# Kernel tuning notes

Measured on AMD Instinct MI355X. Metric: run time of the kernel, lower is better.

Reference implementation:

```python
import jax, jax.numpy as jnp
import numpy as np

NEG_SLOPE = 0.2

def leaky(x):
    return jnp.where(x >= 0, x, NEG_SLOPE * x)

def setup_inputs() -> dict:
    key = jax.random.key(0)
    ks = jax.random.split(key, 9)
    B, D, H = 2048, 128, 512
    s = lambda fan: 1.0 / np.sqrt(fan)
    return {
        "x":   jax.random.normal(ks[0], (B, D), jnp.float32),
        "We1": jax.random.normal(ks[1], (H, D), jnp.float32) * s(D),
        "be1": jax.random.normal(ks[2], (H,), jnp.float32) * s(D),
        "We2": jax.random.normal(ks[3], (D, H), jnp.float32) * s(H),
        "be2": jax.random.normal(ks[4], (D,), jnp.float32) * s(H),
        "W1s": jax.random.normal(ks[5], (D, H), jnp.float32),      # dec_j.linear1 weight (H,1) stacked -> (D,H)
        "b1s": jax.random.normal(ks[6], (D, H), jnp.float32) * 0.1,
        "W2s": jax.random.normal(ks[7], (D, D, H), jnp.float32) * s(H),  # dec_j.linear2 weight (D,H) stacked
        "b2s": jax.random.normal(ks[8], (D, D), jnp.float32) * s(H),
    }

def reference(x, We1, be1, We2, be2, W1s, b1s, W2s, b2s):
    # Encoder: D -> H -> D, tanh
    enc_h = leaky(x @ We1.T + be1)                     # (B,H)
    encoded = jnp.tanh(enc_h @ We2.T + be2)            # (B,D)
    # Per-feature decoders, vectorized over j: dec_j(encoded[:, j])
    z = encoded.T                                      # (D,B) latent scalar per decoder j
    hid = leaky(z[:, :, None] * W1s[:, None, :] + b1s[:, None, :])   # (D,B,H)
    terms = jnp.einsum('jbh,jdh->jbd', hid, W2s) + b2s[:, None, :]   # (D,B,D)
    # outputs[i] = sum_{j<=i} terms[j] -> inclusive prefix sum over j
    outputs = jnp.tanh(jnp.cumsum(terms, axis=0))      # (D,B,D)
    return outputs
```

## Files before the change

### kernel.cpp

```cpp
#include <hip/hip_runtime.h>

#define B_SZ 2048
#define D_SZ 128
#define H_SZ 512
#define JC 8
#define NCH 16
#define CPG 3
#define NGRP 5

typedef _Float16 half8 __attribute__((ext_vector_type(8)));
typedef float floatx4 __attribute__((ext_vector_type(4)));
typedef unsigned int uint4v __attribute__((ext_vector_type(4)));

static __device__ __forceinline__ float tanh_fast(float x) {
  float e = __expf(2.0f * x);
  return 1.0f - 2.0f * __builtin_amdgcn_rcpf(e + 1.0f);
}

static __device__ __forceinline__ void split_pair(float a, float b,
                                                  unsigned int& hi,
                                                  unsigned int& lo) {
  auto h = __builtin_amdgcn_cvt_pkrtz(a, b);
  float ra = a - (float)h[0];
  float rb = b - (float)h[1];
  auto l = __builtin_amdgcn_cvt_pkrtz(ra, rb);
  hi = __builtin_bit_cast(unsigned int, h);
  lo = __builtin_bit_cast(unsigned int, l);
}

__global__ __launch_bounds__(256) void split_w2_kernel(
    const float* __restrict__ W2s, _Float16* __restrict__ W2h,
    _Float16* __restrict__ W2l) {
  const int idx = blockIdx.x * 256 + threadIdx.x;
  const int dl = idx & 63, kg = (idx >> 6) & 63, dtj = idx >> 12;
  const int d = (dtj & 1) * 64 + dl, j = dtj >> 1;
  const float* src = W2s + ((size_t)j * D_SZ + d) * H_SZ + kg * 8;
  float4 a = *(const float4*)src;
  float4 b = *(const float4*)(src + 4);
  unsigned int h0, l0, h1, l1, h2, l2, h3, l3;
  split_pair(a.x, a.y, h0, l0); split_pair(a.z, a.w, h1, l1);
  split_pair(b.x, b.y, h2, l2); split_pair(b.z, b.w, h3, l3);
  ((uint4*)W2h)[idx] = make_uint4(h0, h1, h2, h3);
  ((uint4*)W2l)[idx] = make_uint4(l0, l1, l2, l3);
}

__global__ __launch_bounds__(256) void enc_kernel(
    const float* __restrict__ x, const float* __restrict__ We1,
    const float* __restrict__ be1, const float* __restrict__ We2,
    const float* __restrict__ be2, float* __restrict__ z) {
  __shared__ float xs[8][132];
  __shared__ float hs[8][516];
  const int t = threadIdx.x;
  const int b0 = blockIdx.x * 8;
  {
    int r = t >> 5, c4 = t & 31;
    float4 v = ((const float4*)(x + (size_t)(b0 + r) * D_SZ))[c4];
    xs[r][c4 * 4 + 0] = v.x; xs[r][c4 * 4 + 1] = v.y;
    xs[r][c4 * 4 + 2] = v.z; xs[r][c4 * 4 + 3] = v.w;
  }
  __syncthreads();
  for (int hb = 0; hb < 2; ++hb) {
    const int h = t + hb * 256;
    float acc[8];
    float bias = be1[h];
#pragma unroll
    for (int r = 0; r < 8; ++r) acc[r] = bias;
    const float4* wp = (const float4*)(We1 + (size_t)h * D_SZ);
    for (int k4 = 0; k4 < 32; ++k4) {
      float4 wv = wp[k4];
#pragma unroll
      for (int r = 0; r < 8; ++r) {
        acc[r] = fmaf(wv.x, xs[r][k4 * 4 + 0], acc[r]);
        acc[r] = fmaf(wv.y, xs[r][k4 * 4 + 1], acc[r]);
        acc[r] = fmaf(wv.z, xs[r][k4 * 4 + 2], acc[r]);
        acc[r] = fmaf(wv.w, xs[r][k4 * 4 + 3], acc[r]);
      }
    }
#pragma unroll
    for (int r = 0; r < 8; ++r) {
      float u = acc[r];
      hs[r][h] = fmaxf(u, 0.2f * u);
    }
  }
  __syncthreads();
  {
    const int d = t & 127, rg = t >> 7;
    float acc[4];
    float bias = be2[d];
#pragma unroll
    for (int r = 0; r < 4; ++r) acc[r] = bias;
    const float4* wp = (const float4*)(We2 + (size_t)d * H_SZ);
    for (int k4 = 0; k4 < 128; ++k4) {
      float4 wv = wp[k4];
#pragma unroll
      for (int r = 0; r < 4; ++r) {
        int row = rg * 4 + r;
        acc[r] = fmaf(wv.x, hs[row][k4 * 4 + 0], acc[r]);
        acc[r] = fmaf(wv.y, hs[row][k4 * 4 + 1], acc[r]);
        acc[r] = fmaf(wv.z, hs[row][k4 * 4 + 2], acc[r]);
        acc[r] = fmaf(wv.w, hs[row][k4 * 4 + 3], acc[r]);
      }
    }
#pragma unroll
    for (int r = 0; r < 4; ++r) {
      z[(size_t)d * B_SZ + b0 + rg * 4 + r] = tanh_fast(acc[r]);
    }
  }
}

__global__ __launch_bounds__(256, 4) void dec_kernel(
    const float* __restrict__ W1s, const float* __restrict__ b1s,
    const _Float16* __restrict__ W2h, const _Float16* __restrict__ W2l,
    const float* __restrict__ b2s, const float* __restrict__ z,
    float* __restrict__ out, float* __restrict__ T) {
  __shared__ float w1L[JC][512];
  __shared__ float b1L[JC][512];
  __shared__ float zL[JC][64];
  __shared__ float b2L[JC][64];

  const int t = threadIdx.x, bx = blockIdx.x;
  const int cohort = bx & 31, bt = bx >> 5;
  const int dt = cohort & 1, jc = cohort >> 1;
  const int b0 = bt * 64, d0 = dt * 64, j0 = jc * JC;

#pragma unroll
  for (int i = 0; i < 4; ++i) {
    int g = t + 256 * i;
    int jr = g >> 7, col = (g & 127) * 4;
    *(float4*)&w1L[jr][col] = *(const float4*)(W1s + (size_t)(j0 + jr) * H_SZ + col);
    *(float4*)&b1L[jr][col] = *(const float4*)(b1s + (size_t)(j0 + jr) * H_SZ + col);
  }
  if (t < 128) {
    int jr = t >> 4, col = (t & 15) * 4;
    *(float4*)&zL[jr][col]  = *(const float4*)(z   + (size_t)(j0 + jr) * B_SZ + b0 + col);
    *(float4*)&b2L[jr][col] = *(const float4*)(b2s + (size_t)(j0 + jr) * D_SZ + d0 + col);
  }
  __syncthreads();

  const int lane = t & 63;
  const int quad = lane >> 4, l16 = lane & 15;
  const int wb = (t >> 6) & 1, wd = t >> 7;
  const int brow0 = wb * 32 + l16;

  floatx4 acc[2][2][3];
#pragma unroll
  for (int a = 0; a < 2; ++a)
#pragma unroll
    for (int b = 0; b < 2; ++b)
#pragma unroll
      for (int p = 0; p < 3; ++p) acc[a][b][p] = (floatx4){0.f, 0.f, 0.f, 0.f};
  float bc0 = 0.f, bc1 = 0.f;

  for (int jj = 0; jj < JC; ++jj) {
    const int j = j0 + jj;
    const size_t bbase = ((size_t)j * 2 + dt) * 32768 + (wd * 32 + l16) * 8;
    const float zv0 = zL[jj][brow0];
    const float zv1 = zL[jj][brow0 + 16];

#pragma unroll 2
    for (int ks = 0; ks < 16; ++ks) {
      const int ko = ks * 32 + quad * 8;
      float4 wa = *(const float4*)&w1L[jj][ko];
      float4 wc = *(const float4*)&w1L[jj][ko + 4];
      float4 ba = *(const float4*)&b1L[jj][ko];
      float4 bb = *(const float4*)&b1L[jj][ko + 4];
      const size_t boff = bbase + (size_t)(ks * 4 + quad) * 512;
      half8 fb0h = *(const half8*)(W2h + boff);
      half8 fb0l = *(const half8*)(W2l + boff);
      half8 fb1h = *(const half8*)(W2h + boff + 128);
      half8 fb1l = *(const half8*)(W2l + boff + 128);

      float h0 = fmaf(zv0, wa.x, ba.x), h1 = fmaf(zv0, wa.y, ba.y);
      float h2 = fmaf(zv0, wa.z, ba.z), h3 = fmaf(zv0, wa.w, ba.w);
      float h4 = fmaf(zv0, wc.x, bb.x), h5 = fmaf(zv0, wc.y, bb.y);
      float h6 = fmaf(zv0, wc.z, bb.z), h7 = fmaf(zv0, wc.w, bb.w);
      h0 = fmaxf(h0, 0.2f * h0); h1 = fmaxf(h1, 0.2f * h1);
      h2 = fmaxf(h2, 0.2f * h2); h3 = fmaxf(h3, 0.2f * h3);
      h4 = fmaxf(h4, 0.2f * h4); h5 = fmaxf(h5, 0.2f * h5);
      h6 = fmaxf(h6, 0.2f * h6); h7 = fmaxf(h7, 0.2f * h7);
      unsigned int a0, a1, a2, a3, x0, x1, x2, x3;
      split_pair(h0, h1, a0, x0); split_pair(h2, h3, a1, x1);
      split_pair(h4, h5, a2, x2); split_pair(h6, h7, a3, x3);
      half8 fa0h = __builtin_bit_cast(half8, (uint4v){a0, a1, a2, a3});
      half8 fa0l = __builtin_bit_cast(half8, (uint4v){x0, x1, x2, x3});
      h0 = fmaf(zv1, wa.x, ba.x); h1 = fmaf(zv1, wa.y, ba.y);
      h2 = fmaf(zv1, wa.z, ba.z); h3 = fmaf(zv1, wa.w, ba.w);
      h4 = fmaf(zv1, wc.x, bb.x); h5 = fmaf(zv1, wc.y, bb.y);
      h6 = fmaf(zv1, wc.z, bb.z); h7 = fmaf(zv1, wc.w, bb.w);
      h0 = fmaxf(h0, 0.2f * h0); h1 = fmaxf(h1, 0.2f * h1);
      h2 = fmaxf(h2, 0.2f * h2); h3 = fmaxf(h3, 0.2f * h3);
      h4 = fmaxf(h4, 0.2f * h4); h5 = fmaxf(h5, 0.2f * h5);
      h6 = fmaxf(h6, 0.2f * h6); h7 = fmaxf(h7, 0.2f * h7);
      split_pair(h0, h1, a0, x0); split_pair(h2, h3, a1, x1);
      split_pair(h4, h5, a2, x2); split_pair(h6, h7, a3, x3);
      half8 fa1h = __builtin_bit_cast(half8, (uint4v){a0, a1, a2, a3});
      half8 fa1l = __builtin_bit_cast(half8, (uint4v){x0, x1, x2, x3});

      acc[0][0][0] = __builtin_amdgcn_mfma_f32_16x16x32_f16(fa0h, fb0h, acc[0][0][0], 0, 0, 0);
      acc[0][0][1] = __builtin_amdgcn_mfma_f32_16x16x32_f16(fa0h, fb0l, acc[0][0][1], 0, 0, 0);
      acc[0][0][2] = __builtin_amdgcn_mfma_f32_16x16x32_f16(fa0l, fb0h, acc[0][0][2], 0, 0, 0);
      acc[0][1][0] = __builtin_amdgcn_mfma_f32_16x16x32_f16(fa0h, fb1h, acc[0][1][0], 0, 0, 0);
      acc[0][1][1] = __builtin_amdgcn_mfma_f32_16x16x32_f16(fa0h, fb1l, acc[0][1][1], 0, 0, 0);
      acc[0][1][2] = __builtin_amdgcn_mfma_f32_16x16x32_f16(fa0l, fb1h, acc[0][1][2], 0, 0, 0);
      acc[1][0][0] = __builtin_amdgcn_mfma_f32_16x16x32_f16(fa1h, fb0h, acc[1][0][0], 0, 0, 0);
      acc[1][0][1] = __builtin_amdgcn_mfma_f32_16x16x32_f16(fa1h, fb0l, acc[1][0][1], 0, 0, 0);
      acc[1][0][2] = __builtin_amdgcn_mfma_f32_16x16x32_f16(fa1l, fb0h, acc[1][0][2], 0, 0, 0);
      acc[1][1][0] = __builtin_amdgcn_mfma_f32_16x16x32_f16(fa1h, fb1h, acc[1][1][0], 0, 0, 0);
      acc[1][1][1] = __builtin_amdgcn_mfma_f32_16x16x32_f16(fa1h, fb1l, acc[1][1][1], 0, 0, 0);
      acc[1][1][2] = __builtin_amdgcn_mfma_f32_16x16x32_f16(fa1l, fb1h, acc[1][1][2], 0, 0, 0);
    }

    bc0 += b2L[jj][wd * 32 + l16];
    bc1 += b2L[jj][wd * 32 + 16 + l16];

    const int dcol = d0 + wd * 32 + l16;
    float* obase = out + (size_t)j * (B_SZ * D_SZ) + dcol;
#pragma unroll
    for (int bf = 0; bf < 2; ++bf) {
      const int brow = b0 + wb * 32 + bf * 16 + quad * 4;
      float* orow = obase + (size_t)brow * D_SZ;
#pragma unroll
      for (int r = 0; r < 4; ++r) {
        float s0 = (acc[bf][0][0][r] + acc[bf][0][1][r]) + (acc[bf][0][2][r] + bc0);
        float s1 = (acc[bf][1][0][r] + acc[bf][1][1][r]) + (acc[bf][1][2][r] + bc1);
        if (jc == 0) { s0 = tanh_fast(s0); s1 = tanh_fast(s1); }
        orow[(size_t)r * D_SZ] = s0;
        orow[(size_t)r * D_SZ + 16] = s1;
      }
    }
  }

  if (jc < NCH - 1) {
    const int dcol = d0 + wd * 32 + l16;
    float* tbase = T + (size_t)jc * (B_SZ * D_SZ) + dcol;
#pragma unroll
    for (int bf = 0; bf < 2; ++bf) {
      const int brow = b0 + wb * 32 + bf * 16 + quad * 4;
      float* trow = tbase + (size_t)brow * D_SZ;
#pragma unroll
      for (int r = 0; r < 4; ++r) {
        trow[(size_t)r * D_SZ] =
            (acc[bf][0][0][r] + acc[bf][0][1][r]) + (acc[bf][0][2][r] + bc0);
        trow[(size_t)r * D_SZ + 16] =
            (acc[bf][1][0][r] + acc[bf][1][1][r]) + (acc[bf][1][2][r] + bc1);
      }
    }
  }
}

__global__ __launch_bounds__(256) void fixup_kernel(
    const float* __restrict__ T, float* __restrict__ out) {
  const int idx = blockIdx.x * 256 + threadIdx.x;
  const int d4 = idx & 31;
  const int b = (idx >> 5) & (B_SZ - 1);
  const int q = idx >> 16;
  const size_t stride = B_SZ * (D_SZ / 4);
  const size_t tix = (size_t)b * (D_SZ / 4) + d4;
  const float4* T4 = (const float4*)T;
  float4* O4 = (float4*)out;

  const int c0 = 1 + q * CPG;
  float4 carry = make_float4(0.f, 0.f, 0.f, 0.f);
  for (int c = 0; c < c0; ++c) {
    float4 tv = T4[(size_t)c * stride + tix];
    carry.x += tv.x; carry.y += tv.y; carry.z += tv.z; carry.w += tv.w;
  }
#pragma unroll
  for (int cc = 0; cc < CPG; ++cc) {
    const int c = c0 + cc;
    if (cc > 0) {
      float4 tv = T4[(size_t)(c - 1) * stride + tix];
      carry.x += tv.x; carry.y += tv.y; carry.z += tv.z; carry.w += tv.w;
    }
#pragma unroll
    for (int jj = 0; jj < JC; ++jj) {
      const int j = c * JC + jj;
      const size_t oix = ((size_t)j * B_SZ + b) * (D_SZ / 4) + d4;
      float4 s = O4[oix];
      s.x = tanh_fast(s.x + carry.x);
      s.y = tanh_fast(s.y + carry.y);
      s.z = tanh_fast(s.z + carry.z);
      s.w = tanh_fast(s.w + carry.w);
      O4[oix] = s;
    }
  }
}

extern "C" void kernel_launch(void* const* d_in, const int* in_sizes, int n_in,
                              void* d_out, int out_size, void* d_ws,
                              size_t ws_size, hipStream_t stream) {
  (void)in_sizes; (void)n_in; (void)out_size; (void)ws_size;
  const float* x   = (const float*)d_in[0];
  const float* We1 = (const float*)d_in[1];
  const float* be1 = (const float*)d_in[2];
  const float* We2 = (const float*)d_in[3];
  const float* be2 = (const float*)d_in[4];
  const float* W1s = (const float*)d_in[5];
  const float* b1s = (const float*)d_in[6];
  const float* W2s = (const float*)d_in[7];
  const float* b2s = (const float*)d_in[8];
  float* out = (float*)d_out;

  float* zws = (float*)d_ws;
  _Float16* W2h = (_Float16*)((char*)d_ws + (1u << 20));
  _Float16* W2l = (_Float16*)((char*)d_ws + (1u << 20) + (1u << 24));
  float* T = (float*)((char*)d_ws + (1u << 20) + (2u << 24));

  split_w2_kernel<<<4096, 256, 0, stream>>>(W2s, W2h, W2l);
  enc_kernel<<<256, 256, 0, stream>>>(x, We1, be1, We2, be2, zws);
  dec_kernel<<<1024, 256, 0, stream>>>(W1s, b1s, W2h, W2l, b2s, zws, out, T);
  fixup_kernel<<<NGRP * 256, 256, 0, stream>>>(T, out);
}
```

Before: 383.4 us.

## Widen decoder block tile to cover all 128 output columns

Each decoder block now covers the full D=128 output width instead of half, so the grid drops from 1024 to 512 blocks and the per-block hidden activation (leaky + fp16 split) is computed once per 128 columns rather than twice. Each wave holds 4 column fragments (24 accumulators) and issues 8 B-fragment loads per k-step, with W2 fragment indexing redone to match the new layout. Launch bounds drop to 2 blocks per CU to fit the larger register footprint. This cuts redundant hidden-layer computation and duplicate W1/b1/z staging, at the cost of lower occupancy and fewer blocks to hide memory latency.

Result: faster. 359.0 us (-6.3%).

```diff
diff --git a/kernel.cpp b/kernel.cpp
--- a/kernel.cpp
+++ b/kernel.cpp
@@ -108,7 +108,7 @@
   }
 }
 
-__global__ __launch_bounds__(256, 4) void dec_kernel(
+__global__ __launch_bounds__(256, 2) void dec_kernel(
     const float* __restrict__ W1s, const float* __restrict__ b1s,
     const _Float16* __restrict__ W2h, const _Float16* __restrict__ W2l,
     const float* __restrict__ b2s, const float* __restrict__ z,
@@ -116,12 +116,11 @@
   __shared__ float w1L[JC][512];
   __shared__ float b1L[JC][512];
   __shared__ float zL[JC][64];
-  __shared__ float b2L[JC][64];
+  __shared__ float b2L[JC][128];
 
   const int t = threadIdx.x, bx = blockIdx.x;
-  const int cohort = bx & 31, bt = bx >> 5;
-  const int dt = cohort & 1, jc = cohort >> 1;
-  const int b0 = bt * 64, d0 = dt * 64, j0 = jc * JC;
+  const int jc = bx & 15, bt = bx >> 4;
+  const int b0 = bt * 64, j0 = jc * JC;
 
 #pragma unroll
   for (int i = 0; i < 4; ++i) {
@@ -132,8 +131,11 @@
   }
   if (t < 128) {
     int jr = t >> 4, col = (t & 15) * 4;
-    *(float4*)&zL[jr][col]  = *(const float4*)(z   + (size_t)(j0 + jr) * B_SZ + b0 + col);
-    *(float4*)&b2L[jr][col] = *(const float4*)(b2s + (size_t)(j0 + jr) * D_SZ + d0 + col);
+    *(float4*)&zL[jr][col] = *(const float4*)(z + (size_t)(j0 + jr) * B_SZ + b0 + col);
+  }
+  {
+    int jr = t >> 5, col = (t & 31) * 4;
+    *(float4*)&b2L[jr][col] = *(const float4*)(b2s + (size_t)(j0 + jr) * D_SZ + col);
   }
   __syncthreads();
 
@@ -142,18 +144,19 @@
   const int wb = (t >> 6) & 1, wd = t >> 7;
   const int brow0 = wb * 32 + l16;
 
-  floatx4 acc[2][2][3];
+  floatx4 acc[2][4][3];
 #pragma unroll
   for (int a = 0; a < 2; ++a)
 #pragma unroll
-    for (int b = 0; b < 2; ++b)
+    for (int b = 0; b < 4; ++b)
 #pragma unroll
       for (int p = 0; p < 3; ++p) acc[a][b][p] = (floatx4){0.f, 0.f, 0.f, 0.f};
-  float bc0 = 0.f, bc1 = 0.f;
+  float bc[4] = {0.f, 0.f, 0.f, 0.f};
 
   for (int jj = 0; jj < JC; ++jj) {
     const int j = j0 + jj;
-    const size_t bbase = ((size_t)j * 2 + dt) * 32768 + (wd * 32 + l16) * 8;
+    const unsigned int bbase =
+        (unsigned)(j * 2 + wd) * 32768u + (unsigned)(quad * 512 + l16 * 8);
     const float zv0 = zL[jj][brow0];
     const float zv1 = zL[jj][brow0 + 16];
 
@@ -164,11 +167,15 @@
       float4 wc = *(const float4*)&w1L[jj][ko + 4];
       float4 ba = *(const float4*)&b1L[jj][ko];
       float4 bb = *(const float4*)&b1L[jj][ko + 4];
-      const size_t boff = bbase + (size_t)(ks * 4 + quad) * 512;
-      half8 fb0h = *(const half8*)(W2h + boff);
-      half8 fb0l = *(const half8*)(W2l + boff);
-      half8 fb1h = *(const half8*)(W2h + boff + 128);
-      half8 fb1l = *(const half8*)(W2l + boff + 128);
+      const unsigned int boff = bbase + (unsigned)(ks * 2048);
+      half8 fbh0 = *(const half8*)(W2h + boff);
+      half8 fbh1 = *(const half8*)(W2h + boff + 128);
+      half8 fbh2 = *(const half8*)(W2h + boff + 256);
+      half8 fbh3 = *(const half8*)(W2h + boff + 384);
+      half8 fbl0 = *(const half8*)(W2l + boff);
+      half8 fbl1 = *(const half8*)(W2l + boff + 128);
+      half8 fbl2 = *(const half8*)(W2l + boff + 256);
+      half8 fbl3 = *(const half8*)(W2l + boff + 384);
 
       float h0 = fmaf(zv0, wa.x, ba.x), h1 = fmaf(zv0, wa.y, ba.y);
       float h2 = fmaf(zv0, wa.z, ba.z), h3 = fmaf(zv0, wa.w, ba.w);
@@ -183,6 +190,20 @@
       split_pair(h4, h5, a2, x2); split_pair(h6, h7, a3, x3);
       half8 fa0h = __builtin_bit_cast(half8, (uint4v){a0, a1, a2, a3});
       half8 fa0l = __builtin_bit_cast(half8, (uint4v){x0, x1, x2, x3});
+
+      acc[0][0][0] = __builtin_amdgcn_mfma_f32_16x16x32_f16(fa0h, fbh0, acc[0][0][0], 0, 0, 0);
+      acc[0][0][1] = __builtin_amdgcn_mfma_f32_16x16x32_f16(fa0h, fbl0, acc[0][0][1], 0, 0, 0);
+      acc[0][0][2] = __builtin_amdgcn_mfma_f32_16x16x32_f16(fa0l, fbh0, acc[0][0][2], 0, 0, 0);
+      acc[0][1][0] = __builtin_amdgcn_mfma_f32_16x16x32_f16(fa0h, fbh1, acc[0][1][0], 0, 0, 0);
+      acc[0][1][1] = __builtin_amdgcn_mfma_f32_16x16x32_f16(fa0h, fbl1, acc[0][1][1], 0, 0, 0);
+      acc[0][1][2] = __builtin_amdgcn_mfma_f32_16x16x32_f16(fa0l, fbh1, acc[0][1][2], 0, 0, 0);
+      acc[0][2][0] = __builtin_amdgcn_mfma_f32_16x16x32_f16(fa0h, fbh2, acc[0][2][0], 0, 0, 0);
+      acc[0][2][1] = __builtin_amdgcn_mfma_f32_16x16x32_f16(fa0h, fbl2, acc[0][2][1], 0, 0, 0);
+      acc[0][2][2] = __builtin_amdgcn_mfma_f32_16x16x32_f16(fa0l, fbh2, acc[0][2][2], 0, 0, 0);
+      acc[0][3][0] = __builtin_amdgcn_mfma_f32_16x16x32_f16(fa0h, fbh3, acc[0][3][0], 0, 0, 0);
+      acc[0][3][1] = __builtin_amdgcn_mfma_f32_16x16x32_f16(fa0h, fbl3, acc[0][3][1], 0, 0, 0);
+      acc[0][3][2] = __builtin_amdgcn_mfma_f32_16x16x32_f16(fa0l, fbh3, acc[0][3][2], 0, 0, 0);
+
       h0 = fmaf(zv1, wa.x, ba.x); h1 = fmaf(zv1, wa.y, ba.y);
       h2 = fmaf(zv1, wa.z, ba.z); h3 = fmaf(zv1, wa.w, ba.w);
       h4 = fmaf(zv1, wc.x, bb.x); h5 = fmaf(zv1, wc.y, bb.y);
@@ -196,24 +217,24 @@
       half8 fa1h = __builtin_bit_cast(half8, (uint4v){a0, a1, a2, a3});
       half8 fa1l = __builtin_bit_cast(half8, (uint4v){x0, x1, x2, x3});
 
-      acc[0][0][0] = __builtin_amdgcn_mfma_f32_16x16x32_f16(fa0h, fb0h, acc[0][0][0], 0, 0, 0);
-      acc[0][0][1] = __builtin_amdgcn_mfma_f32_16x16x32_f16(fa0h, fb0l, acc[0][0][1], 0, 0, 0);
-      acc[0][0][2] = __builtin_amdgcn_mfma_f32_16x16x32_f16(fa0l, fb0h, acc[0][0][2], 0, 0, 0);
-      acc[0][1][0] = __builtin_amdgcn_mfma_f32_16x16x32_f16(fa0h, fb1h, acc[0][1][0], 0, 0, 0);
-      acc[0][1][1] = __builtin_amdgcn_mfma_f32_16x16x32_f16(fa0h, fb1l, acc[0][1][1], 0, 0, 0);
-      acc[0][1][2] = __builtin_amdgcn_mfma_f32_16x16x32_f16(fa0l, fb1h, acc[0][1][2], 0, 0, 0);
-      acc[1][0][0] = __builtin_amdgcn_mfma_f32_16x16x32_f16(fa1h, fb0h, acc[1][0][0], 0, 0, 0);
-      acc[1][0][1] = __builtin_amdgcn_mfma_f32_16x16x32_f16(fa1h, fb0l, acc[1][0][1], 0, 0, 0);
-      acc[1][0][2] = __builtin_amdgcn_mfma_f32_16x16x32_f16(fa1l, fb0h, acc[1][0][2], 0, 0, 0);
-      acc[1][1][0] = __builtin_amdgcn_mfma_f32_16x16x32_f16(fa1h, fb1h, acc[1][1][0], 0, 0, 0);
-      acc[1][1][1] = __builtin_amdgcn_mfma_f32_16x16x32_f16(fa1h, fb1l, acc[1][1][1], 0, 0, 0);
-      acc[1][1][2] = __builtin_amdgcn_mfma_f32_16x16x32_f16(fa1l, fb1h, acc[1][1][2], 0, 0, 0);
-    }
-
-    bc0 += b2L[jj][wd * 32 + l16];
-    bc1 += b2L[jj][wd * 32 + 16 + l16];
-
-    const int dcol = d0 + wd * 32 + l16;
+      acc[1][0][0] = __builtin_amdgcn_mfma_f32_16x16x32_f16(fa1h, fbh0, acc[1][0][0], 0, 0, 0);
+      acc[1][0][1] = __builtin_amdgcn_mfma_f32_16x16x32_f16(fa1h, fbl0, acc[1][0][1], 0, 0, 0);
+      acc[1][0][2] = __builtin_amdgcn_mfma_f32_16x16x32_f16(fa1l, fbh0, acc[1][0][2], 0, 0, 0);
+      acc[1][1][0] = __builtin_amdgcn_mfma_f32_16x16x32_f16(fa1h, fbh1, acc[1][1][0], 0, 0, 0);
+      acc[1][1][1] = __builtin_amdgcn_mfma_f32_16x16x32_f16(fa1h, fbl1, acc[1][1][1], 0, 0, 0);
+      acc[1][1][2] = __builtin_amdgcn_mfma_f32_16x16x32_f16(fa1l, fbh1, acc[1][1][2], 0, 0, 0);
+      acc[1][2][0] = __builtin_amdgcn_mfma_f32_16x16x32_f16(fa1h, fbh2, acc[1][2][0], 0, 0, 0);
+      acc[1][2][1] = __builtin_amdgcn_mfma_f32_16x16x32_f16(fa1h, fbl2, acc[1][2][1], 0, 0, 0);
+      acc[1][2][2] = __builtin_amdgcn_mfma_f32_16x16x32_f16(fa1l, fbh2, acc[1][2][2], 0, 0, 0);
+      acc[1][3][0] = __builtin_amdgcn_mfma_f32_16x16x32_f16(fa1h, fbh3, acc[1][3][0], 0, 0, 0);
+      acc[1][3][1] = __builtin_amdgcn_mfma_f32_16x16x32_f16(fa1h, fbl3, acc[1][3][1], 0, 0, 0);
+      acc[1][3][2] = __builtin_amdgcn_mfma_f32_16x16x32_f16(fa1l, fbh3, acc[1][3][2], 0, 0, 0);
+    }
+
+#pragma unroll
+    for (int df = 0; df < 4; ++df) bc[df] += b2L[jj][wd * 64 + df * 16 + l16];
+
+    const int dcol = wd * 64 + l16;
     float* obase = out + (size_t)j * (B_SZ * D_SZ) + dcol;
 #pragma unroll
     for (int bf = 0; bf < 2; ++bf) {
@@ -221,17 +242,19 @@
       float* orow = obase + (size_t)brow * D_SZ;
 #pragma unroll
       for (int r = 0; r < 4; ++r) {
-        float s0 = (acc[bf][0][0][r] + acc[bf][0][1][r]) + (acc[bf][0][2][r] + bc0);
-        float s1 = (acc[bf][1][0][r] + acc[bf][1][1][r]) + (acc[bf][1][2][r] + bc1);
-        if (jc == 0) { s0 = tanh_fast(s0); s1 = tanh_fast(s1); }
-        orow[(size_t)r * D_SZ] = s0;
-        orow[(size_t)r * D_SZ + 16] = s1;
+#pragma unroll
+        for (int df = 0; df < 4; ++df) {
+          float s = (acc[bf][df][0][r] + acc[bf][df][1][r]) +
+                    (acc[bf][df][2][r] + bc[df]);
+          if (jc == 0) s = tanh_fast(s);
+          orow[(size_t)r * D_SZ + df * 16] = s;
+        }
       }
     }
   }
 
   if (jc < NCH - 1) {
-    const int dcol = d0 + wd * 32 + l16;
+    const int dcol = wd * 64 + l16;
     float* tbase = T + (size_t)jc * (B_SZ * D_SZ) + dcol;
 #pragma unroll
     for (int bf = 0; bf < 2; ++bf) {
@@ -239,10 +262,12 @@
       float* trow = tbase + (size_t)brow * D_SZ;
 #pragma unroll
       for (int r = 0; r < 4; ++r) {
-        trow[(size_t)r * D_SZ] =
-            (acc[bf][0][0][r] + acc[bf][0][1][r]) + (acc[bf][0][2][r] + bc0);
-        trow[(size_t)r * D_SZ + 16] =
-            (acc[bf][1][0][r] + acc[bf][1][1][r]) + (acc[bf][1][2][r] + bc1);
+#pragma unroll
+        for (int df = 0; df < 4; ++df) {
+          trow[(size_t)r * D_SZ + df * 16] =
+              (acc[bf][df][0][r] + acc[bf][df][1][r]) +
+              (acc[bf][df][2][r] + bc[df]);
+        }
       }
     }
   }
@@ -308,6 +333,6 @@
 
   split_w2_kernel<<<4096, 256, 0, stream>>>(W2s, W2h, W2l);
   enc_kernel<<<256, 256, 0, stream>>>(x, We1, be1, We2, be2, zws);
-  dec_kernel<<<1024, 256, 0, stream>>>(W1s, b1s, W2h, W2l, b2s, zws, out, T);
+  dec_kernel<<<512, 256, 0, stream>>>(W1s, b1s, W2h, W2l, b2s, zws, out, T);
   fixup_kernel<<<NGRP * 256, 256, 0, stream>>>(T, out);
 }
```

## Widen decoder tiles to full D per block and fuse encoder with weight split

Applied to the files above, without the earlier changes.

The decoder block now covers all 128 output columns for 64 batch rows, with each wave handling 16 rows across eight d-fragments. The hidden activation computation and fp16 split are therefore done once per batch fragment instead of being duplicated across two d-tiles, and the grid halves. The encoder and W2 split kernels are merged into one launch to remove a launch boundary. The cost is more accumulator registers per thread (occupancy hint lowered to 2) and more global B-fragment loads per iteration.

Measured after the change: 368.7 us. 3.8% less time.

```diff
diff --git a/kernel.cpp b/kernel.cpp
--- a/kernel.cpp
+++ b/kernel.cpp
@@ -28,29 +28,29 @@
   lo = __builtin_bit_cast(unsigned int, l);
 }
 
-__global__ __launch_bounds__(256) void split_w2_kernel(
+__global__ __launch_bounds__(256) void prep_kernel(
     const float* __restrict__ W2s, _Float16* __restrict__ W2h,
-    _Float16* __restrict__ W2l) {
-  const int idx = blockIdx.x * 256 + threadIdx.x;
-  const int dl = idx & 63, kg = (idx >> 6) & 63, dtj = idx >> 12;
-  const int d = (dtj & 1) * 64 + dl, j = dtj >> 1;
-  const float* src = W2s + ((size_t)j * D_SZ + d) * H_SZ + kg * 8;
-  float4 a = *(const float4*)src;
-  float4 b = *(const float4*)(src + 4);
-  unsigned int h0, l0, h1, l1, h2, l2, h3, l3;
-  split_pair(a.x, a.y, h0, l0); split_pair(a.z, a.w, h1, l1);
-  split_pair(b.x, b.y, h2, l2); split_pair(b.z, b.w, h3, l3);
-  ((uint4*)W2h)[idx] = make_uint4(h0, h1, h2, h3);
-  ((uint4*)W2l)[idx] = make_uint4(l0, l1, l2, l3);
-}
-
-__global__ __launch_bounds__(256) void enc_kernel(
-    const float* __restrict__ x, const float* __restrict__ We1,
-    const float* __restrict__ be1, const float* __restrict__ We2,
-    const float* __restrict__ be2, float* __restrict__ z) {
+    _Float16* __restrict__ W2l, const float* __restrict__ x,
+    const float* __restrict__ We1, const float* __restrict__ be1,
+    const float* __restrict__ We2, const float* __restrict__ be2,
+    float* __restrict__ z) {
+  const int t = threadIdx.x;
+  if (blockIdx.x >= 256) {
+    const int idx = (blockIdx.x - 256) * 256 + t;
+    const int dl = idx & 63, kg = (idx >> 6) & 63, dtj = idx >> 12;
+    const int d = (dtj & 1) * 64 + dl, j = dtj >> 1;
+    const float* src = W2s + ((size_t)j * D_SZ + d) * H_SZ + kg * 8;
+    float4 a = *(const float4*)src;
+    float4 b = *(const float4*)(src + 4);
+    unsigned int h0, l0, h1, l1, h2, l2, h3, l3;
+    split_pair(a.x, a.y, h0, l0); split_pair(a.z, a.w, h1, l1);
+    split_pair(b.x, b.y, h2, l2); split_pair(b.z, b.w, h3, l3);
+    ((uint4*)W2h)[idx] = make_uint4(h0, h1, h2, h3);
+    ((uint4*)W2l)[idx] = make_uint4(l0, l1, l2, l3);
+    return;
+  }
   __shared__ float xs[8][132];
   __shared__ float hs[8][516];
-  const int t = threadIdx.x;
   const int b0 = blockIdx.x * 8;
   {
     int r = t >> 5, c4 = t & 31;
@@ -108,7 +108,7 @@
   }
 }
 
-__global__ __launch_bounds__(256, 4) void dec_kernel(
+__global__ __launch_bounds__(256, 2) void dec_kernel(
     const float* __restrict__ W1s, const float* __restrict__ b1s,
     const _Float16* __restrict__ W2h, const _Float16* __restrict__ W2l,
     const float* __restrict__ b2s, const float* __restrict__ z,
@@ -116,12 +116,11 @@
   __shared__ float w1L[JC][512];
   __shared__ float b1L[JC][512];
   __shared__ float zL[JC][64];
-  __shared__ float b2L[JC][64];
+  __shared__ float b2L[JC][128];
 
   const int t = threadIdx.x, bx = blockIdx.x;
-  const int cohort = bx & 31, bt = bx >> 5;
-  const int dt = cohort & 1, jc = cohort >> 1;
-  const int b0 = bt * 64, d0 = dt * 64, j0 = jc * JC;
+  const int jc = bx & 15, bt = bx >> 4;
+  const int b0 = bt * 64, j0 = jc * JC;
 
 #pragma unroll
   for (int i = 0; i < 4; ++i) {
@@ -132,30 +131,31 @@
   }
   if (t < 128) {
     int jr = t >> 4, col = (t & 15) * 4;
-    *(float4*)&zL[jr][col]  = *(const float4*)(z   + (size_t)(j0 + jr) * B_SZ + b0 + col);
-    *(float4*)&b2L[jr][col] = *(const float4*)(b2s + (size_t)(j0 + jr) * D_SZ + d0 + col);
+    *(float4*)&zL[jr][col] = *(const float4*)(z + (size_t)(j0 + jr) * B_SZ + b0 + col);
+  }
+  {
+    int jr = t >> 5, col = (t & 31) * 4;
+    *(float4*)&b2L[jr][col] = *(const float4*)(b2s + (size_t)(j0 + jr) * D_SZ + col);
   }
   __syncthreads();
 
   const int lane = t & 63;
   const int quad = lane >> 4, l16 = lane & 15;
-  const int wb = (t >> 6) & 1, wd = t >> 7;
-  const int brow0 = wb * 32 + l16;
-
-  floatx4 acc[2][2][3];
-#pragma unroll
-  for (int a = 0; a < 2; ++a)
-#pragma unroll
-    for (int b = 0; b < 2; ++b)
-#pragma unroll
-      for (int p = 0; p < 3; ++p) acc[a][b][p] = (floatx4){0.f, 0.f, 0.f, 0.f};
-  float bc0 = 0.f, bc1 = 0.f;
+  const int w = t >> 6;
+  const int brow0 = w * 16 + l16;
+
+  floatx4 acc[8][3];
+#pragma unroll
+  for (int d = 0; d < 8; ++d)
+#pragma unroll
+    for (int p = 0; p < 3; ++p) acc[d][p] = (floatx4){0.f, 0.f, 0.f, 0.f};
+  float bc[8] = {0.f, 0.f, 0.f, 0.f, 0.f, 0.f, 0.f, 0.f};
 
   for (int jj = 0; jj < JC; ++jj) {
     const int j = j0 + jj;
-    const size_t bbase = ((size_t)j * 2 + dt) * 32768 + (wd * 32 + l16) * 8;
-    const float zv0 = zL[jj][brow0];
-    const float zv1 = zL[jj][brow0 + 16];
+    const unsigned int bb0 =
+        (unsigned)(j * 2) * 32768u + (unsigned)(quad * 512 + l16 * 8);
+    const float zv = zL[jj][brow0];
 
 #pragma unroll 2
     for (int ks = 0; ks < 16; ++ks) {
@@ -164,16 +164,29 @@
       float4 wc = *(const float4*)&w1L[jj][ko + 4];
       float4 ba = *(const float4*)&b1L[jj][ko];
       float4 bb = *(const float4*)&b1L[jj][ko + 4];
-      const size_t boff = bbase + (size_t)(ks * 4 + quad) * 512;
-      half8 fb0h = *(const half8*)(W2h + boff);
-      half8 fb0l = *(const half8*)(W2l + boff);
-      half8 fb1h = *(const half8*)(W2h + boff + 128);
-      half8 fb1l = *(const half8*)(W2l + boff + 128);
-
-      float h0 = fmaf(zv0, wa.x, ba.x), h1 = fmaf(zv0, wa.y, ba.y);
-      float h2 = fmaf(zv0, wa.z, ba.z), h3 = fmaf(zv0, wa.w, ba.w);
-      float h4 = fmaf(zv0, wc.x, bb.x), h5 = fmaf(zv0, wc.y, bb.y);
-      float h6 = fmaf(zv0, wc.z, bb.z), h7 = fmaf(zv0, wc.w, bb.w);
+      const unsigned int off0 = bb0 + (unsigned)(ks * 2048);
+      const unsigned int off1 = off0 + 32768u;
+      half8 fh0 = *(const half8*)(W2h + off0);
+      half8 fh1 = *(const half8*)(W2h + off0 + 128);
+      half8 fh2 = *(const half8*)(W2h + off0 + 256);
+      half8 fh3 = *(const half8*)(W2h + off0 + 384);
+      half8 gh0 = *(const half8*)(W2h + off1);
+      half8 gh1 = *(const half8*)(W2h + off1 + 128);
+      half8 gh2 = *(const half8*)(W2h + off1 + 256);
+      half8 gh3 = *(const half8*)(W2h + off1 + 384);
+      half8 fl0 = *(const half8*)(W2l + off0);
+      half8 fl1 = *(const half8*)(W2l + off0 + 128);
+      half8 fl2 = *(const half8*)(W2l + off0 + 256);
+      half8 fl3 = *(const half8*)(W2l + off0 + 384);
+      half8 gl0 = *(const half8*)(W2l + off1);
+      half8 gl1 = *(const half8*)(W2l + off1 + 128);
+      half8 gl2 = *(const half8*)(W2l + off1 + 256);
+      half8 gl3 = *(const half8*)(W2l + off1 + 384);
+
+      float h0 = fmaf(zv, wa.x, ba.x), h1 = fmaf(zv, wa.y, ba.y);
+      float h2 = fmaf(zv, wa.z, ba.z), h3 = fmaf(zv, wa.w, ba.w);
+      float h4 = fmaf(zv, wc.x, bb.x), h5 = fmaf(zv, wc.y, bb.y);
+      float h6 = fmaf(zv, wc.z, bb.z), h7 = fmaf(zv, wc.w, bb.w);
       h0 = fmaxf(h0, 0.2f * h0); h1 = fmaxf(h1, 0.2f * h1);
       h2 = fmaxf(h2, 0.2f * h2); h3 = fmaxf(h3, 0.2f * h3);
       h4 = fmaxf(h4, 0.2f * h4); h5 = fmaxf(h5, 0.2f * h5);
@@ -181,68 +194,62 @@
       unsigned int a0, a1, a2, a3, x0, x1, x2, x3;
       split_pair(h0, h1, a0, x0); split_pair(h2, h3, a1, x1);
       split_pair(h4, h5, a2, x2); split_pair(h6, h7, a3, x3);
-      half8 fa0h = __builtin_bit_cast(half8, (uint4v){a0, a1, a2, a3});
-      half8 fa0l = __builtin_bit_cast(half8, (uint4v){x0, x1, x2, x3});
-      h0 = fmaf(zv1, wa.x, ba.x); h1 = fmaf(zv1, wa.y, ba.y);
-      h2 = fmaf(zv1, wa.z, ba.z); h3 = fmaf(zv1, wa.w, ba.w);
-      h4 = fmaf(zv1, wc.x, bb.x); h5 = fmaf(zv1, wc.y, bb.y);
-      h6 = fmaf(zv1, wc.z, bb.z); h7 = fmaf(zv1, wc.w, bb.w);
-      h0 = fmaxf(h0, 0.2f * h0); h1 = fmaxf(h1, 0.2f * h1);
-      h2 = fmaxf(h2, 0.2f * h2); h3 = fmaxf(h3, 0.2f * h3);
-      h4 = fmaxf(h4, 0.2f * h4); h5 = fmaxf(h5, 0.2f * h5);
-      h6 = fmaxf(h6, 0.2f * h6); h7 = fmaxf(h7, 0.2f * h7);
-      split_pair(h0, h1, a0, x0); split_pair(h2, h3, a1, x1);
-      split_pair(h4, h5, a2, x2); split_pair(h6, h7, a3, x3);
-      half8 fa1h = __builtin_bit_cast(half8, (uint4v){a0, a1, a2, a3});
-      half8 fa1l = __builtin_bit_cast(half8, (uint4v){x0, x1, x2, x3});
-
-      acc[0][0][0] = __builtin_amdgcn_mfma_f32_16x16x32_f16(fa0h, fb0h, acc[0][0][0], 0, 0, 0);
-      acc[0][0][1] = __builtin_amdgcn_mfma_f32_16x16x32_f16(fa0h, fb0l, acc[0][0][1], 0, 0, 0);
-      acc[0][0][2] = __builtin_amdgcn_mfma_f32_16x16x32_f16(fa0l, fb0h, acc[0][0][2], 0, 0, 0);
-      acc[0][1][0] = __builtin_amdgcn_mfma_f32_16x16x32_f16(fa0h, fb1h, acc[0][1][0], 0, 0, 0);
-      acc[0][1][1] = __builtin_amdgcn_mfma_f32_16x16x32_f16(fa0h, fb1l, acc[0][1][1], 0, 0, 0);
-      acc[0][1][2] = __builtin_amdgcn_mfma_f32_16x16x32_f16(fa0l, fb1h, acc[0][1][2], 0, 0, 0);
-      acc[1][0][0] = __builtin_amdgcn_mfma_f32_16x16x32_f16(fa1h, fb0h, acc[1][0][0], 0, 0, 0);
-      acc[1][0][1] = __builtin_amdgcn_mfma_f32_16x16x32_f16(fa1h, fb0l, acc[1][0][1], 0, 0, 0);
-      acc[1][0][2] = __builtin_amdgcn_mfma_f32_16x16x32_f16(fa1l, fb0h, acc[1][0][2], 0, 0, 0);
-      acc[1][1][0] = __builtin_amdgcn_mfma_f32_16x16x32_f16(fa1h, fb1h, acc[1][1][0], 0, 0, 0);
-      acc[1][1][1] = __builtin_amdgcn_mfma_f32_16x16x32_f16(fa1h, fb1l, acc[1][1][1], 0, 0, 0);
-      acc[1][1][2] = __builtin_amdgcn_mfma_f32_16x16x32_f16(fa1l, fb1h, acc[1][1][2], 0, 0, 0);
-    }
-
-    bc0 += b2L[jj][wd * 32 + l16];
-    bc1 += b2L[jj][wd * 32 + 16 + l16];
-
-    const int dcol = d0 + wd * 32 + l16;
-    float* obase = out + (size_t)j * (B_SZ * D_SZ) + dcol;
-#pragma unroll
-    for (int bf = 0; bf < 2; ++bf) {
-      const int brow = b0 + wb * 32 + bf * 16 + quad * 4;
-      float* orow = obase + (size_t)brow * D_SZ;
-#pragma unroll
-      for (int r = 0; r < 4; ++r) {
-        float s0 = (acc[bf][0][0][r] + acc[bf][0][1][r]) + (acc[bf][0][2][r] + bc0);
-        float s1 = (acc[bf][1][0][r] + acc[bf][1][1][r]) + (acc[bf][1][2][r] + bc1);
-        if (jc == 0) { s0 = tanh_fast(s0); s1 = tanh_fast(s1); }
-        orow[(size_t)r * D_SZ] = s0;
-        orow[(size_t)r * D_SZ + 16] = s1;
+      half8 fah = __builtin_bit_cast(half8, (uint4v){a0, a1, a2, a3});
+      half8 fal = __builtin_bit_cast(half8, (uint4v){x0, x1, x2, x3});
+
+      acc[0][0] = __builtin_amdgcn_mfma_f32_16x16x32_f16(fah, fh0, acc[0][0], 0, 0, 0);
+      acc[0][1] = __builtin_amdgcn_mfma_f32_16x16x32_f16(fah, fl0, acc[0][1], 0, 0, 0);
+      acc[0][2] = __builtin_amdgcn_mfma_f32_16x16x32_f16(fal, fh0, acc[0][2], 0, 0, 0);
+      acc[1][0] = __builtin_amdgcn_mfma_f32_16x16x32_f16(fah, fh1, acc[1][0], 0, 0, 0);
+      acc[1][1] = __builtin_amdgcn_mfma_f32_16x16x32_f16(fah, fl1, acc[1][1], 0, 0, 0);
+      acc[1][2] = __builtin_amdgcn_mfma_f32_16x16x32_f16(fal, fh1, acc[1][2], 0, 0, 0);
+      acc[2][0] = __builtin_amdgcn_mfma_f32_16x16x32_f16(fah, fh2, acc[2][0], 0, 0, 0);
+      acc[2][1] = __builtin_amdgcn_mfma_f32_16x16x32_f16(fah, fl2, acc[2][1], 0, 0, 0);
+      acc[2][2] = __builtin_amdgcn_mfma_f32_16x16x32_f16(fal, fh2, acc[2][2], 0, 0, 0);
+      acc[3][0] = __builtin_amdgcn_mfma_f32_16x16x32_f16(fah, fh3, acc[3][0], 0, 0, 0);
+      acc[3][1] = __builtin_amdgcn_mfma_f32_16x16x32_f16(fah, fl3, acc[3][1], 0, 0, 0);
+      acc[3][2] = __builtin_amdgcn_mfma_f32_16x16x32_f16(fal, fh3, acc[3][2], 0, 0, 0);
+      acc[4][0] = __builtin_amdgcn_mfma_f32_16x16x32_f16(fah, gh0, acc[4][0], 0, 0, 0);
+      acc[4][1] = __builtin_amdgcn_mfma_f32_16x16x32_f16(fah, gl0, acc[4][1], 0, 0, 0);
+      acc[4][2] = __builtin_amdgcn_mfma_f32_16x16x32_f16(fal, gh0, acc[4][2], 0, 0, 0);
+      acc[5][0] = __builtin_amdgcn_mfma_f32_16x16x32_f16(fah, gh1, acc[5][0], 0, 0, 0);
+      acc[5][1] = __builtin_amdgcn_mfma_f32_16x16x32_f16(fah, gl1, acc[5][1], 0, 0, 0);
+      acc[5][2] = __builtin_amdgcn_mfma_f32_16x16x32_f16(fal, gh1, acc[5][2], 0, 0, 0);
+      acc[6][0] = __builtin_amdgcn_mfma_f32_16x16x32_f16(fah, gh2, acc[6][0], 0, 0, 0);
+      acc[6][1] = __builtin_amdgcn_mfma_f32_16x16x32_f16(fah, gl2, acc[6][1], 0, 0, 0);
+      acc[6][2] = __builtin_amdgcn_mfma_f32_16x16x32_f16(fal, gh2, acc[6][2], 0, 0, 0);
+      acc[7][0] = __builtin_amdgcn_mfma_f32_16x16x32_f16(fah, gh3, acc[7][0], 0, 0, 0);
+      acc[7][1] = __builtin_amdgcn_mfma_f32_16x16x32_f16(fah, gl3, acc[7][1], 0, 0, 0);
+      acc[7][2] = __builtin_amdgcn_mfma_f32_16x16x32_f16(fal, gh3, acc[7][2], 0, 0, 0);
+    }
+
+#pragma unroll
+    for (int df = 0; df < 8; ++df) bc[df] += b2L[jj][df * 16 + l16];
+
+    float* obase = out + (size_t)j * (B_SZ * D_SZ) + l16;
+    const int brow = b0 + w * 16 + quad * 4;
+    float* orow0 = obase + (size_t)brow * D_SZ;
+#pragma unroll
+    for (int r = 0; r < 4; ++r) {
+#pragma unroll
+      for (int df = 0; df < 8; ++df) {
+        float s = (acc[df][0][r] + acc[df][1][r]) + (acc[df][2][r] + bc[df]);
+        if (jc == 0) s = tanh_fast(s);
+        orow0[(size_t)r * D_SZ + df * 16] = s;
       }
     }
   }
 
   if (jc < NCH - 1) {
-    const int dcol = d0 + wd * 32 + l16;
-    float* tbase = T + (size_t)jc * (B_SZ * D_SZ) + dcol;
-#pragma unroll
-    for (int bf = 0; bf < 2; ++bf) {
-      const int brow = b0 + wb * 32 + bf * 16 + quad * 4;
-      float* trow = tbase + (size_t)brow * D_SZ;
-#pragma unroll
-      for (int r = 0; r < 4; ++r) {
-        trow[(size_t)r * D_SZ] =
-            (acc[bf][0][0][r] + acc[bf][0][1][r]) + (acc[bf][0][2][r] + bc0);
-        trow[(size_t)r * D_SZ + 16] =
-            (acc[bf][1][0][r] + acc[bf][1][1][r]) + (acc[bf][1][2][r] + bc1);
+    float* tbase = T + (size_t)jc * (B_SZ * D_SZ) + l16;
+    const int brow = b0 + w * 16 + quad * 4;
+    float* trow0 = tbase + (size_t)brow * D_SZ;
+#pragma unroll
+    for (int r = 0; r < 4; ++r) {
+#pragma unroll
+      for (int df = 0; df < 8; ++df) {
+        trow0[(size_t)r * D_SZ + df * 16] =
+            (acc[df][0][r] + acc[df][1][r]) + (acc[df][2][r] + bc[df]);
       }
     }
   }
@@ -306,8 +313,7 @@
   _Float16* W2l = (_Float16*)((char*)d_ws + (1u << 20) + (1u << 24));
   float* T = (float*)((char*)d_ws + (1u << 20) + (2u << 24));
 
-  split_w2_kernel<<<4096, 256, 0, stream>>>(W2s, W2h, W2l);
-  enc_kernel<<<256, 256, 0, stream>>>(x, We1, be1, We2, be2, zws);
-  dec_kernel<<<1024, 256, 0, stream>>>(W1s, b1s, W2h, W2l, b2s, zws, out, T);
+  prep_kernel<<<4352, 256, 0, stream>>>(W2s, W2h, W2l, x, We1, be1, We2, be2, zws);
+  dec_kernel<<<512, 256, 0, stream>>>(W1s, b1s, W2h, W2l, b2s, zws, out, T);
   fixup_kernel<<<NGRP * 256, 256, 0, stream>>>(T, out);
 }
```
